# Kernel tuning notes

Measured on AMD Instinct MI355X. Metric: run time of the kernel, lower is better.

Reference implementation:

```python
import jax, jax.numpy as jnp
import numpy as np
import math

B, L, S = 2, 2048, 2048
DIN, DK, DV, DOUT, H = 512, 512, 512, 512, 8
HEAD_SIZE = DK / H  # attention_head_size = dim_key_query_all / num_attention_heads


def setup_inputs() -> dict:
    key = jax.random.key(0)
    ks = jax.random.split(key, 12)
    inv = 1.0 / math.sqrt(DIN)
    return {
        "queries": jax.random.normal(ks[0], (B, L, DIN), jnp.float32),
        "keys": jax.random.normal(ks[1], (B, S, DIN), jnp.float32),
        "values": jax.random.normal(ks[2], (B, S, DIN), jnp.float32),
        "attn_mask": 0,
        "Wq": jax.random.uniform(ks[3], (DK, DIN), jnp.float32, -inv, inv),
        "Wk": jax.random.uniform(ks[4], (DK, DIN), jnp.float32, -inv, inv),
        "Wv": jax.random.uniform(ks[5], (DV, DIN), jnp.float32, -inv, inv),
        "bv": jax.random.uniform(ks[6], (DV,), jnp.float32, -inv, inv),
        "Wcb": jax.random.uniform(ks[7], (H, DIN), jnp.float32, -inv, inv),
        "mixing": 0.2 * jax.random.normal(ks[8], (H, DK), jnp.float32),
        "Wd": jax.random.uniform(ks[9], (DOUT, DV), jnp.float32, -1.0 / math.sqrt(DV), 1.0 / math.sqrt(DV)),
        "bd": jax.random.uniform(ks[10], (DOUT,), jnp.float32, -1.0 / math.sqrt(DV), 1.0 / math.sqrt(DV)),
    }


def reference(queries, keys, values, attn_mask, Wq, Wk, Wv, bv, Wcb, mixing, Wd, bd):
    # projections
    q = jnp.einsum('bld,ed->ble', queries, Wq)            # [B,L,DK]
    k = jnp.einsum('bsd,ed->bse', keys, Wk)               # [B,S,DK]
    v = jnp.einsum('bsd,ed->bse', values, Wv) + bv        # [B,S,DV]
    v = v.reshape(B, S, H, DV // H).transpose(0, 2, 1, 3)  # [B,H,S,dv]
    # collaborative scores: (q * mixing_h) @ k^T, per head
    mixed_q = q[:, None, :, :] * mixing[None, :, None, :]  # [B,H,L,DK]
    scores = jnp.einsum('bhle,bse->bhls', mixed_q, k)      # [B,H,L,S]
    # content bias: keys -> [B,S,H] -> broadcast over queries
    cb = jnp.einsum('bsd,hd->bhs', keys, Wcb)              # [B,H,S]
    scores = (scores + cb[:, :, None, :]) / math.sqrt(HEAD_SIZE)
    probs = jax.nn.softmax(scores, axis=-1)                # dropout p=0 (eval)
    ctx = jnp.einsum('bhls,bhsv->bhlv', probs, v)          # [B,H,L,dv]
    ctx = ctx.transpose(0, 2, 1, 3).reshape(B, L, DV)      # [B,L,DV]
    out = jnp.einsum('blv,ov->blo', ctx, Wd) + bd          # [B,L,DOUT]
    return out, probs
```

## Files before the change

### kernel.cpp

```cpp
#include <hip/hip_runtime.h>

typedef unsigned short u16;
typedef __bf16 bf16x8 __attribute__((ext_vector_type(8)));
typedef float floatx4 __attribute__((ext_vector_type(4)));

#define B_ 2
#define L_ 2048
#define S_ 2048
#define D_ 512
#define H_ 8

static __device__ __forceinline__ u16 f2bf(float f) {
  union { float f; unsigned u; } v; v.f = f;
  unsigned u = v.u;
  return (u16)((u + 0x7FFFu + ((u >> 16) & 1u)) >> 16);
}
static __device__ __forceinline__ float bf2f(u16 h) {
  union { unsigned u; float f; } v; v.u = ((unsigned)h) << 16;
  return v.f;
}

static __device__ __forceinline__ void gload16(const void* g, void* l) {
  __builtin_amdgcn_global_load_lds(
      (const __attribute__((address_space(1))) void*)g,
      (__attribute__((address_space(3))) void*)l, 16, 0, 0);
}

__global__ __launch_bounds__(256) void qkv_gemm(
    const float* __restrict__ Qin, const float* __restrict__ Kin, const float* __restrict__ Vin,
    const float* __restrict__ Wq, const float* __restrict__ Wk, const float* __restrict__ Wv,
    const float* __restrict__ bv,
    u16* __restrict__ qo, u16* __restrict__ ko, u16* __restrict__ vo)
{
  __shared__ u16 As[128][72];
  __shared__ u16 Bs[128][72];
  const int z = blockIdx.z;
  const float* A = (z == 0) ? Qin : (z == 1) ? Kin : Vin;
  const float* W = (z == 0) ? Wq : (z == 1) ? Wk : Wv;
  const int tid = threadIdx.x;
  const int m0 = blockIdx.y * 128;
  const int n0 = blockIdx.x * 128;
  const int lane = tid & 63, w = tid >> 6;
  const int ml = lane & 15, kl = lane >> 4;
  const int mqw = (w >> 1) * 64, nq = (w & 1) * 64;
  const int srow = tid >> 4, scg = tid & 15;

  floatx4 acc[4][4] = {};

  for (int k0 = 0; k0 < 512; k0 += 64) {
#pragma unroll
    for (int i = 0; i < 8; ++i) {
      const int r = srow + i * 16;
      float4 av = *(const float4*)&A[(size_t)(m0 + r) * 512 + k0 + scg * 4];
      ushort4 ua; ua.x = f2bf(av.x); ua.y = f2bf(av.y); ua.z = f2bf(av.z); ua.w = f2bf(av.w);
      *(ushort4*)&As[r][scg * 4] = ua;
      float4 wv = *(const float4*)&W[(size_t)(n0 + r) * 512 + k0 + scg * 4];
      ushort4 uw; uw.x = f2bf(wv.x); uw.y = f2bf(wv.y); uw.z = f2bf(wv.z); uw.w = f2bf(wv.w);
      *(ushort4*)&Bs[r][scg * 4] = uw;
    }
    __syncthreads();
#pragma unroll
    for (int kk = 0; kk < 64; kk += 32) {
      bf16x8 af[4], bfv[4];
#pragma unroll
      for (int i = 0; i < 4; ++i) af[i] = *(const bf16x8*)&As[mqw + i * 16 + ml][kk + kl * 8];
#pragma unroll
      for (int j = 0; j < 4; ++j) bfv[j] = *(const bf16x8*)&Bs[nq + j * 16 + ml][kk + kl * 8];
#pragma unroll
      for (int i = 0; i < 4; ++i)
#pragma unroll
        for (int j = 0; j < 4; ++j)
          acc[i][j] = __builtin_amdgcn_mfma_f32_16x16x32_bf16(af[i], bfv[j], acc[i][j], 0, 0, 0);
    }
    __syncthreads();
  }
#pragma unroll
  for (int i = 0; i < 4; ++i)
#pragma unroll
    for (int j = 0; j < 4; ++j) {
      const int gc = n0 + nq + j * 16 + ml;
#pragma unroll
      for (int r = 0; r < 4; ++r) {
        const int gr = m0 + mqw + i * 16 + kl * 4 + r;
        float v = acc[i][j][r];
        if (z == 0)      qo[(size_t)gr * 512 + gc] = f2bf(v);
        else if (z == 1) ko[(size_t)gr * 512 + gc] = f2bf(v);
        else             vo[(size_t)gr * 512 + gc] = f2bf(v + bv[gc]);
      }
    }
}

__global__ __launch_bounds__(256) void mixq_kernel(
    const u16* __restrict__ qb, const float* __restrict__ mixing, u16* __restrict__ mq)
{
  __shared__ float mixs[8 * 512];
  const int tid = threadIdx.x;
#pragma unroll
  for (int i = 0; i < 4; ++i)
    *(float4*)&mixs[(tid + i * 256) * 4] = *(const float4*)&mixing[(tid + i * 256) * 4];
  __syncthreads();
  const size_t unit = (size_t)blockIdx.x * 256 + tid;
  const size_t el = unit * 8;
  const int e = (int)(el & 511);
  const size_t bl = el >> 9;
  const int b = (int)(bl >> 11);
  const int l = (int)(bl & 2047);
  uint4 qv = *(const uint4*)&qb[el];
  const float q0 = bf2f((u16)(qv.x & 0xFFFFu)), q1 = bf2f((u16)(qv.x >> 16));
  const float q2 = bf2f((u16)(qv.y & 0xFFFFu)), q3 = bf2f((u16)(qv.y >> 16));
  const float q4 = bf2f((u16)(qv.z & 0xFFFFu)), q5 = bf2f((u16)(qv.z >> 16));
  const float q6 = bf2f((u16)(qv.w & 0xFFFFu)), q7 = bf2f((u16)(qv.w >> 16));
#pragma unroll
  for (int h = 0; h < 8; ++h) {
    const float* mp = &mixs[h * 512 + e];
    uint4 o;
    o.x = (unsigned)f2bf(q0 * mp[0]) | ((unsigned)f2bf(q1 * mp[1]) << 16);
    o.y = (unsigned)f2bf(q2 * mp[2]) | ((unsigned)f2bf(q3 * mp[3]) << 16);
    o.z = (unsigned)f2bf(q4 * mp[4]) | ((unsigned)f2bf(q5 * mp[5]) << 16);
    o.w = (unsigned)f2bf(q6 * mp[6]) | ((unsigned)f2bf(q7 * mp[7]) << 16);
    *(uint4*)&mq[(((size_t)b * 8 + h) * 2048 + l) * 512 + e] = o;
  }
}

__global__ __launch_bounds__(256) void out_gemm(
    const float* __restrict__ A, const float* __restrict__ W,
    const float* __restrict__ bias, float* __restrict__ out)
{
  __shared__ u16 As[128][72];
  __shared__ u16 Bs[128][72];
  const int tid = threadIdx.x;
  const int m0 = blockIdx.y * 128;
  const int n0 = blockIdx.x * 128;
  const int lane = tid & 63, w = tid >> 6;
  const int ml = lane & 15, kl = lane >> 4;
  const int mqw = (w >> 1) * 64, nq = (w & 1) * 64;
  const int srow = tid >> 4, scg = tid & 15;

  floatx4 acc[4][4] = {};

  for (int k0 = 0; k0 < 512; k0 += 64) {
#pragma unroll
    for (int i = 0; i < 8; ++i) {
      const int r = srow + i * 16;
      float4 av = *(const float4*)&A[(size_t)(m0 + r) * 512 + k0 + scg * 4];
      ushort4 ua; ua.x = f2bf(av.x); ua.y = f2bf(av.y); ua.z = f2bf(av.z); ua.w = f2bf(av.w);
      *(ushort4*)&As[r][scg * 4] = ua;
      float4 wv = *(const float4*)&W[(size_t)(n0 + r) * 512 + k0 + scg * 4];
      ushort4 uw; uw.x = f2bf(wv.x); uw.y = f2bf(wv.y); uw.z = f2bf(wv.z); uw.w = f2bf(wv.w);
      *(ushort4*)&Bs[r][scg * 4] = uw;
    }
    __syncthreads();
#pragma unroll
    for (int kk = 0; kk < 64; kk += 32) {
      bf16x8 af[4], bfv[4];
#pragma unroll
      for (int i = 0; i < 4; ++i) af[i] = *(const bf16x8*)&As[mqw + i * 16 + ml][kk + kl * 8];
#pragma unroll
      for (int j = 0; j < 4; ++j) bfv[j] = *(const bf16x8*)&Bs[nq + j * 16 + ml][kk + kl * 8];
#pragma unroll
      for (int i = 0; i < 4; ++i)
#pragma unroll
        for (int j = 0; j < 4; ++j)
          acc[i][j] = __builtin_amdgcn_mfma_f32_16x16x32_bf16(af[i], bfv[j], acc[i][j], 0, 0, 0);
    }
    __syncthreads();
  }
#pragma unroll
  for (int i = 0; i < 4; ++i)
#pragma unroll
    for (int j = 0; j < 4; ++j) {
      const int gc = n0 + nq + j * 16 + ml;
#pragma unroll
      for (int r = 0; r < 4; ++r) {
        const int gr = m0 + mqw + i * 16 + kl * 4 + r;
        out[(size_t)gr * 512 + gc] = acc[i][j][r] + bias[gc];
      }
    }
}

__global__ __launch_bounds__(256) void cb_kernel(
    const float* __restrict__ keys, const float* __restrict__ Wcb, float* __restrict__ cbuf)
{
  __shared__ float Wl[8 * 512];
  const int tid = threadIdx.x;
#pragma unroll
  for (int i = 0; i < 4; ++i) {
    const int idx = tid + i * 256;
    *(float4*)&Wl[idx * 4] = *(const float4*)&Wcb[idx * 4];
  }
  __syncthreads();
  const int w = tid >> 6, lane = tid & 63;
  const int rowid = blockIdx.x * 4 + w;
  const int b = rowid >> 11, s = rowid & 2047;
  const float* kr = keys + (size_t)rowid * 512;
  float acc[8] = {0.f, 0.f, 0.f, 0.f, 0.f, 0.f, 0.f, 0.f};
  for (int e = lane; e < 512; e += 64) {
    const float kv = kr[e];
#pragma unroll
    for (int hh = 0; hh < 8; ++hh) acc[hh] += kv * Wl[hh * 512 + e];
  }
#pragma unroll
  for (int hh = 0; hh < 8; ++hh) {
#pragma unroll
    for (int off = 32; off > 0; off >>= 1) acc[hh] += __shfl_xor(acc[hh], off, 64);
  }
  if (lane == 0) {
#pragma unroll
    for (int hh = 0; hh < 8; ++hh)
      cbuf[((size_t)b * 8 + hh) * 2048 + s] = acc[hh];
  }
}

__global__ __launch_bounds__(256) void transpose_v(
    const u16* __restrict__ vb, u16* __restrict__ vT)
{
  __shared__ u16 t[64][72];
  const int tid = threadIdx.x;
  const int e0 = blockIdx.x * 64;
  const int s0 = blockIdx.y * 64;
  const int b = blockIdx.z;
  const int rr = tid >> 3, g = tid & 7;
#pragma unroll
  for (int i = 0; i < 2; ++i) {
    const int r = rr + i * 32;
    *(uint4*)&t[r][g * 8] = *(const uint4*)&vb[((size_t)b * S_ + s0 + r) * 512 + e0 + g * 8];
  }
  __syncthreads();
#pragma unroll
  for (int i = 0; i < 2; ++i) {
    const int er = rr + i * 32;
    uint4 o;
    o.x = (unsigned)t[g * 8 + 0][er] | ((unsigned)t[g * 8 + 1][er] << 16);
    o.y = (unsigned)t[g * 8 + 2][er] | ((unsigned)t[g * 8 + 3][er] << 16);
    o.z = (unsigned)t[g * 8 + 4][er] | ((unsigned)t[g * 8 + 5][er] << 16);
    o.w = (unsigned)t[g * 8 + 6][er] | ((unsigned)t[g * 8 + 7][er] << 16);
    *(uint4*)&vT[((size_t)b * 512 + e0 + er) * S_ + s0 + g * 8] = o;
  }
}

template<int BF16OUT>
__global__ __launch_bounds__(256) void scores_gemm(
    const u16* __restrict__ mq, const u16* __restrict__ kb,
    const float* __restrict__ cbuf, float* __restrict__ sc, u16* __restrict__ sb)
{
  __shared__ u16 As[128][64];
  __shared__ u16 Bs[128][64];
  const int tid = threadIdx.x;
  const int bh = blockIdx.z, b = bh >> 3;
  const int m0 = blockIdx.y * 128;
  const int n0 = blockIdx.x * 128;
  const u16* mqb = mq + (size_t)bh * L_ * 512;
  const u16* kbb = kb + (size_t)b * S_ * 512;
  const int lane = tid & 63, w = tid >> 6;
  const int ml = lane & 15, kl = lane >> 4;
  const int mqw = (w >> 1) * 64, nq = (w & 1) * 64;
  const int lr = lane >> 3;
  const int lc = (lane & 7) * 8;

  floatx4 acc[4][4] = {};

  for (int k0 = 0; k0 < 512; k0 += 64) {
#pragma unroll
    for (int i = 0; i < 4; ++i) {
      const int c = w * 4 + i;
      const int r = c * 8 + lr;
      gload16(&mqb[(size_t)(m0 + r) * 512 + k0 + lc], &As[c * 8][0]);
      gload16(&kbb[(size_t)(n0 + r) * 512 + k0 + lc], &Bs[c * 8][0]);
    }
    __syncthreads();
#pragma unroll
    for (int kk = 0; kk < 64; kk += 32) {
      bf16x8 af[4], bfv[4];
#pragma unroll
      for (int i = 0; i < 4; ++i) af[i] = *(const bf16x8*)&As[mqw + i * 16 + ml][kk + kl * 8];
#pragma unroll
      for (int j = 0; j < 4; ++j) bfv[j] = *(const bf16x8*)&Bs[nq + j * 16 + ml][kk + kl * 8];
#pragma unroll
      for (int i = 0; i < 4; ++i)
#pragma unroll
        for (int j = 0; j < 4; ++j)
          acc[i][j] = __builtin_amdgcn_mfma_f32_16x16x32_bf16(af[i], bfv[j], acc[i][j], 0, 0, 0);
    }
    __syncthreads();
  }
  if constexpr (BF16OUT) {
    u16* outp = sb + ((size_t)bh * L_ + m0) * S_ + n0;
#pragma unroll
    for (int j = 0; j < 4; ++j) {
      const int gcl = nq + j * 16 + ml;
      const float cbv = cbuf[(size_t)bh * S_ + n0 + gcl];
#pragma unroll
      for (int i = 0; i < 4; ++i)
#pragma unroll
        for (int r = 0; r < 4; ++r) {
          const int grl = mqw + i * 16 + kl * 4 + r;
          outp[(size_t)grl * S_ + gcl] = f2bf((acc[i][j][r] + cbv) * 0.125f);
        }
    }
  } else {
    float* outp = sc + ((size_t)bh * L_ + m0) * S_ + n0;
#pragma unroll
    for (int j = 0; j < 4; ++j) {
      const int gcl = nq + j * 16 + ml;
      const float cbv = cbuf[(size_t)bh * S_ + n0 + gcl];
#pragma unroll
      for (int i = 0; i < 4; ++i)
#pragma unroll
        for (int r = 0; r < 4; ++r) {
          const int grl = mqw + i * 16 + kl * 4 + r;
          outp[(size_t)grl * S_ + gcl] = (acc[i][j][r] + cbv) * 0.125f;
        }
    }
  }
}

template<int BF16IN>
__global__ __launch_bounds__(256) void softmax_stream(
    u16* __restrict__ sb, float* probs)
{
  const int tid = threadIdx.x;
  const int row = blockIdx.x * 4 + (tid >> 6);
  const int lane = tid & 63;
  float s[32];
  if constexpr (BF16IN) {
    const u16* rp = sb + (size_t)row * 2048;
#pragma unroll
    for (int j = 0; j < 8; ++j) {
      uint2 v = *(const uint2*)&rp[lane * 4 + j * 256];
      s[4 * j + 0] = bf2f((u16)(v.x & 0xFFFFu));
      s[4 * j + 1] = bf2f((u16)(v.x >> 16));
      s[4 * j + 2] = bf2f((u16)(v.y & 0xFFFFu));
      s[4 * j + 3] = bf2f((u16)(v.y >> 16));
    }
  } else {
    const float* rp = probs + (size_t)row * 2048;
#pragma unroll
    for (int j = 0; j < 8; ++j) {
      float4 v = *(const float4*)&rp[lane * 4 + j * 256];
      s[4 * j + 0] = v.x; s[4 * j + 1] = v.y; s[4 * j + 2] = v.z; s[4 * j + 3] = v.w;
    }
  }
  float m = -3.0e38f;
#pragma unroll
  for (int i = 0; i < 32; ++i) m = fmaxf(m, s[i]);
#pragma unroll
  for (int off = 32; off > 0; off >>= 1) m = fmaxf(m, __shfl_xor(m, off, 64));
  float s0 = 0.f, s1 = 0.f, s2 = 0.f, s3 = 0.f;
#pragma unroll
  for (int i = 0; i < 32; i += 4) {
    s[i + 0] = __expf(s[i + 0] - m); s0 += s[i + 0];
    s[i + 1] = __expf(s[i + 1] - m); s1 += s[i + 1];
    s[i + 2] = __expf(s[i + 2] - m); s2 += s[i + 2];
    s[i + 3] = __expf(s[i + 3] - m); s3 += s[i + 3];
  }
  float sum = (s0 + s1) + (s2 + s3);
#pragma unroll
  for (int off = 32; off > 0; off >>= 1) sum += __shfl_xor(sum, off, 64);
  const float rl = 1.0f / sum;
  float* op = probs + (size_t)row * 2048;
  u16* bp = sb + (size_t)row * 2048;
#pragma unroll
  for (int j = 0; j < 8; ++j) {
    float4 o;
    o.x = s[4 * j + 0] * rl; o.y = s[4 * j + 1] * rl;
    o.z = s[4 * j + 2] * rl; o.w = s[4 * j + 3] * rl;
    *(float4*)&op[lane * 4 + j * 256] = o;
    if constexpr (BF16IN) {
      uint2 t;
      t.x = (unsigned)f2bf(o.x) | ((unsigned)f2bf(o.y) << 16);
      t.y = (unsigned)f2bf(o.z) | ((unsigned)f2bf(o.w) << 16);
      *(uint2*)&bp[lane * 4 + j * 256] = t;
    }
  }
}

template<int BF16IN>
__global__ __launch_bounds__(256) void ctx_gemm(
    const float* __restrict__ probsf, const u16* __restrict__ pb,
    const u16* __restrict__ vT, float* __restrict__ ctx)
{
  __shared__ u16 As[64][64];
  __shared__ u16 Bs[64][64];
  const int tid = threadIdx.x;
  const int bh = blockIdx.y, b = bh >> 3, h = bh & 7;
  const int m0 = blockIdx.x * 64;
  const int lane = tid & 63, w = tid >> 6;
  const int ml = lane & 15, kl = lane >> 4;
  const int lr = lane >> 3;
  const int lc = (lane & 7) * 8;
  const u16* Ap = pb + ((size_t)bh * L_ + m0) * S_;
  const u16* Bp = vT + ((size_t)b * 512 + h * 64) * S_;

  floatx4 acc[4] = {};

  for (int k0 = 0; k0 < 2048; k0 += 64) {
    if constexpr (BF16IN) {
#pragma unroll
      for (int i = 0; i < 2; ++i) {
        const int c = w * 2 + i;
        const int r = c * 8 + lr;
        gload16(&Ap[(size_t)r * S_ + k0 + lc], &As[c * 8][0]);
        gload16(&Bp[(size_t)r * S_ + k0 + lc], &Bs[c * 8][0]);
      }
    } else {
      const int srow = tid >> 4, scg = tid & 15;
#pragma unroll
      for (int i = 0; i < 4; ++i) {
        const int r = srow + i * 16;
        float4 av = *(const float4*)&probsf[((size_t)bh * L_ + m0 + r) * S_ + k0 + scg * 4];
        ushort4 ua; ua.x = f2bf(av.x); ua.y = f2bf(av.y); ua.z = f2bf(av.z); ua.w = f2bf(av.w);
        *(ushort4*)&As[r][scg * 4] = ua;
      }
#pragma unroll
      for (int i = 0; i < 2; ++i) {
        const int c = w * 2 + i;
        const int r = c * 8 + lr;
        gload16(&Bp[(size_t)r * S_ + k0 + lc], &Bs[c * 8][0]);
      }
    }
    __syncthreads();
#pragma unroll
    for (int kk = 0; kk < 64; kk += 32) {
      bf16x8 af = *(const bf16x8*)&As[w * 16 + ml][kk + kl * 8];
#pragma unroll
      for (int j = 0; j < 4; ++j) {
        bf16x8 bfv = *(const bf16x8*)&Bs[j * 16 + ml][kk + kl * 8];
        acc[j] = __builtin_amdgcn_mfma_f32_16x16x32_bf16(af, bfv, acc[j], 0, 0, 0);
      }
    }
    __syncthreads();
  }
#pragma unroll
  for (int j = 0; j < 4; ++j) {
    const int gc = h * 64 + j * 16 + ml;
#pragma unroll
    for (int r = 0; r < 4; ++r) {
      const int gl = m0 + w * 16 + kl * 4 + r;
      ctx[((size_t)b * L_ + gl) * 512 + gc] = acc[j][r];
    }
  }
}

extern "C" void kernel_launch(void* const* d_in, const int* in_sizes, int n_in,
                              void* d_out, int out_size, void* d_ws, size_t ws_size,
                              hipStream_t stream) {
  const float* queries = (const float*)d_in[0];
  const float* keys    = (const float*)d_in[1];
  const float* values  = (const float*)d_in[2];
  const float* Wq  = (const float*)d_in[4];
  const float* Wk  = (const float*)d_in[5];
  const float* Wv  = (const float*)d_in[6];
  const float* bv  = (const float*)d_in[7];
  const float* Wcb = (const float*)d_in[8];
  const float* mixing = (const float*)d_in[9];
  const float* Wd  = (const float*)d_in[10];
  const float* bd  = (const float*)d_in[11];

  float* out   = (float*)d_out;
  float* probs = out + (size_t)B_ * L_ * 512;

  char* ws = (char*)d_ws;
  u16*   qb  = (u16*)(ws);
  u16*   kb  = (u16*)(ws + (size_t)4  * 1024 * 1024);
  u16*   vb  = (u16*)(ws + (size_t)8  * 1024 * 1024);
  u16*   vT  = (u16*)(ws + (size_t)12 * 1024 * 1024);
  float* cbuf= (float*)(ws + (size_t)16 * 1024 * 1024);
  float* ctx = (float*)(ws + (size_t)17 * 1024 * 1024);
  u16*   mq  = (u16*)(ws + (size_t)25 * 1024 * 1024);
  const size_t SB16_OFF = (size_t)57 * 1024 * 1024;
  const size_t SB16_SZ  = (size_t)B_ * H_ * L_ * S_ * 2;
  u16* sb16 = (u16*)(ws + SB16_OFF);
  const bool bigws = (ws_size >= SB16_OFF + SB16_SZ);

  hipLaunchKernelGGL(qkv_gemm, dim3(4, 32, 3), dim3(256), 0, stream,
                     queries, keys, values, Wq, Wk, Wv, bv, qb, kb, vb);
  hipLaunchKernelGGL(mixq_kernel, dim3(1024), dim3(256), 0, stream, qb, mixing, mq);
  hipLaunchKernelGGL(cb_kernel, dim3(1024), dim3(256), 0, stream, keys, Wcb, cbuf);
  hipLaunchKernelGGL(transpose_v, dim3(8, 32, 2), dim3(256), 0, stream, vb, vT);
  if (bigws) {
    hipLaunchKernelGGL(HIP_KERNEL_NAME(scores_gemm<1>), dim3(16, 16, 16), dim3(256), 0, stream,
                       mq, kb, cbuf, probs, sb16);
    hipLaunchKernelGGL(HIP_KERNEL_NAME(softmax_stream<1>), dim3(8192), dim3(256), 0, stream,
                       sb16, probs);
    hipLaunchKernelGGL(HIP_KERNEL_NAME(ctx_gemm<1>), dim3(32, 16), dim3(256), 0, stream,
                       probs, sb16, vT, ctx);
  } else {
    hipLaunchKernelGGL(HIP_KERNEL_NAME(scores_gemm<0>), dim3(16, 16, 16), dim3(256), 0, stream,
                       mq, kb, cbuf, probs, sb16);
    hipLaunchKernelGGL(HIP_KERNEL_NAME(softmax_stream<0>), dim3(8192), dim3(256), 0, stream,
                       sb16, probs);
    hipLaunchKernelGGL(HIP_KERNEL_NAME(ctx_gemm<0>), dim3(32, 16), dim3(256), 0, stream,
                       probs, sb16, vT, ctx);
  }
  hipLaunchKernelGGL(out_gemm, dim3(4, 32, 1), dim3(256), 0, stream,
                     ctx, Wd, bd, out);
}
```

Before: 579.6 us.

## Split-K the context GEMM and fuse content-bias with V transpose

The probs·V GEMM is split into two K-halves over a new grid dimension, doubling the block count. Each half writes its own partial context buffer, and the output GEMM sums the two partials while staging its A tile. The content-bias kernel and the V transpose kernel are merged into one launch that branches on block index, removing one launch. In exchange the bf16 path now needs an extra 8 MB of workspace, and if the workspace is too small it falls back to the fp32 path.

```diff
diff --git a/kernel.cpp b/kernel.cpp
--- a/kernel.cpp
+++ b/kernel.cpp
@@ -123,7 +123,8 @@
 }
 
 __global__ __launch_bounds__(256) void out_gemm(
-    const float* __restrict__ A, const float* __restrict__ W,
+    const float* __restrict__ A0, const float* __restrict__ A1,
+    const float* __restrict__ W,
     const float* __restrict__ bias, float* __restrict__ out)
 {
   __shared__ u16 As[128][72];
@@ -142,8 +143,12 @@
 #pragma unroll
     for (int i = 0; i < 8; ++i) {
       const int r = srow + i * 16;
-      float4 av = *(const float4*)&A[(size_t)(m0 + r) * 512 + k0 + scg * 4];
-      ushort4 ua; ua.x = f2bf(av.x); ua.y = f2bf(av.y); ua.z = f2bf(av.z); ua.w = f2bf(av.w);
+      const size_t aoff = (size_t)(m0 + r) * 512 + k0 + scg * 4;
+      float4 a0 = *(const float4*)&A0[aoff];
+      float4 a1 = *(const float4*)&A1[aoff];
+      ushort4 ua;
+      ua.x = f2bf(a0.x + a1.x); ua.y = f2bf(a0.y + a1.y);
+      ua.z = f2bf(a0.z + a1.z); ua.w = f2bf(a0.w + a1.w);
       *(ushort4*)&As[r][scg * 4] = ua;
       float4 wv = *(const float4*)&W[(size_t)(n0 + r) * 512 + k0 + scg * 4];
       ushort4 uw; uw.x = f2bf(wv.x); uw.y = f2bf(wv.y); uw.z = f2bf(wv.z); uw.w = f2bf(wv.w);
@@ -178,63 +183,63 @@
     }
 }
 
-__global__ __launch_bounds__(256) void cb_kernel(
-    const float* __restrict__ keys, const float* __restrict__ Wcb, float* __restrict__ cbuf)
+__global__ __launch_bounds__(256) void prep_kernel(
+    const float* __restrict__ keys, const float* __restrict__ Wcb, float* __restrict__ cbuf,
+    const u16* __restrict__ vb, u16* __restrict__ vT)
 {
   __shared__ float Wl[8 * 512];
-  const int tid = threadIdx.x;
-#pragma unroll
-  for (int i = 0; i < 4; ++i) {
-    const int idx = tid + i * 256;
-    *(float4*)&Wl[idx * 4] = *(const float4*)&Wcb[idx * 4];
-  }
-  __syncthreads();
-  const int w = tid >> 6, lane = tid & 63;
-  const int rowid = blockIdx.x * 4 + w;
-  const int b = rowid >> 11, s = rowid & 2047;
-  const float* kr = keys + (size_t)rowid * 512;
-  float acc[8] = {0.f, 0.f, 0.f, 0.f, 0.f, 0.f, 0.f, 0.f};
-  for (int e = lane; e < 512; e += 64) {
-    const float kv = kr[e];
-#pragma unroll
-    for (int hh = 0; hh < 8; ++hh) acc[hh] += kv * Wl[hh * 512 + e];
-  }
-#pragma unroll
-  for (int hh = 0; hh < 8; ++hh) {
-#pragma unroll
-    for (int off = 32; off > 0; off >>= 1) acc[hh] += __shfl_xor(acc[hh], off, 64);
-  }
-  if (lane == 0) {
-#pragma unroll
-    for (int hh = 0; hh < 8; ++hh)
-      cbuf[((size_t)b * 8 + hh) * 2048 + s] = acc[hh];
-  }
-}
-
-__global__ __launch_bounds__(256) void transpose_v(
-    const u16* __restrict__ vb, u16* __restrict__ vT)
-{
   __shared__ u16 t[64][72];
   const int tid = threadIdx.x;
-  const int e0 = blockIdx.x * 64;
-  const int s0 = blockIdx.y * 64;
-  const int b = blockIdx.z;
-  const int rr = tid >> 3, g = tid & 7;
-#pragma unroll
-  for (int i = 0; i < 2; ++i) {
-    const int r = rr + i * 32;
-    *(uint4*)&t[r][g * 8] = *(const uint4*)&vb[((size_t)b * S_ + s0 + r) * 512 + e0 + g * 8];
-  }
-  __syncthreads();
-#pragma unroll
-  for (int i = 0; i < 2; ++i) {
-    const int er = rr + i * 32;
-    uint4 o;
-    o.x = (unsigned)t[g * 8 + 0][er] | ((unsigned)t[g * 8 + 1][er] << 16);
-    o.y = (unsigned)t[g * 8 + 2][er] | ((unsigned)t[g * 8 + 3][er] << 16);
-    o.z = (unsigned)t[g * 8 + 4][er] | ((unsigned)t[g * 8 + 5][er] << 16);
-    o.w = (unsigned)t[g * 8 + 6][er] | ((unsigned)t[g * 8 + 7][er] << 16);
-    *(uint4*)&vT[((size_t)b * 512 + e0 + er) * S_ + s0 + g * 8] = o;
+  if (blockIdx.x < 1024) {
+#pragma unroll
+    for (int i = 0; i < 4; ++i) {
+      const int idx = tid + i * 256;
+      *(float4*)&Wl[idx * 4] = *(const float4*)&Wcb[idx * 4];
+    }
+    __syncthreads();
+    const int w = tid >> 6, lane = tid & 63;
+    const int rowid = blockIdx.x * 4 + w;
+    const int b = rowid >> 11, s = rowid & 2047;
+    const float* kr = keys + (size_t)rowid * 512;
+    float acc[8] = {0.f, 0.f, 0.f, 0.f, 0.f, 0.f, 0.f, 0.f};
+    for (int e = lane; e < 512; e += 64) {
+      const float kv = kr[e];
+#pragma unroll
+      for (int hh = 0; hh < 8; ++hh) acc[hh] += kv * Wl[hh * 512 + e];
+    }
+#pragma unroll
+    for (int hh = 0; hh < 8; ++hh) {
+#pragma unroll
+      for (int off = 32; off > 0; off >>= 1) acc[hh] += __shfl_xor(acc[hh], off, 64);
+    }
+    if (lane == 0) {
+#pragma unroll
+      for (int hh = 0; hh < 8; ++hh)
+        cbuf[((size_t)b * 8 + hh) * 2048 + s] = acc[hh];
+    }
+  } else {
+    const int id = blockIdx.x - 1024;
+    const int b = id >> 8;
+    const int rem = id & 255;
+    const int s0 = (rem >> 3) * 64;
+    const int e0 = (rem & 7) * 64;
+    const int rr = tid >> 3, g = tid & 7;
+#pragma unroll
+    for (int i = 0; i < 2; ++i) {
+      const int r = rr + i * 32;
+      *(uint4*)&t[r][g * 8] = *(const uint4*)&vb[((size_t)b * S_ + s0 + r) * 512 + e0 + g * 8];
+    }
+    __syncthreads();
+#pragma unroll
+    for (int i = 0; i < 2; ++i) {
+      const int er = rr + i * 32;
+      uint4 o;
+      o.x = (unsigned)t[g * 8 + 0][er] | ((unsigned)t[g * 8 + 1][er] << 16);
+      o.y = (unsigned)t[g * 8 + 2][er] | ((unsigned)t[g * 8 + 3][er] << 16);
+      o.z = (unsigned)t[g * 8 + 4][er] | ((unsigned)t[g * 8 + 5][er] << 16);
+      o.w = (unsigned)t[g * 8 + 6][er] | ((unsigned)t[g * 8 + 7][er] << 16);
+      *(uint4*)&vT[((size_t)b * 512 + e0 + er) * S_ + s0 + g * 8] = o;
+    }
   }
 }
 
@@ -377,12 +382,13 @@
 template<int BF16IN>
 __global__ __launch_bounds__(256) void ctx_gemm(
     const float* __restrict__ probsf, const u16* __restrict__ pb,
-    const u16* __restrict__ vT, float* __restrict__ ctx)
+    const u16* __restrict__ vT, float* __restrict__ ctx0, float* __restrict__ ctx1)
 {
   __shared__ u16 As[64][64];
   __shared__ u16 Bs[64][64];
   const int tid = threadIdx.x;
-  const int bh = blockIdx.y, b = bh >> 3, h = bh & 7;
+  const int kz = blockIdx.y;
+  const int bh = blockIdx.z, b = bh >> 3, h = bh & 7;
   const int m0 = blockIdx.x * 64;
   const int lane = tid & 63, w = tid >> 6;
   const int ml = lane & 15, kl = lane >> 4;
@@ -393,7 +399,8 @@
 
   floatx4 acc[4] = {};
 
-  for (int k0 = 0; k0 < 2048; k0 += 64) {
+  const int kend = kz * 1024 + 1024;
+  for (int k0 = kz * 1024; k0 < kend; k0 += 64) {
     if constexpr (BF16IN) {
 #pragma unroll
       for (int i = 0; i < 2; ++i) {
@@ -430,13 +437,14 @@
     }
     __syncthreads();
   }
+  float* cdst = kz ? ctx1 : ctx0;
 #pragma unroll
   for (int j = 0; j < 4; ++j) {
     const int gc = h * 64 + j * 16 + ml;
 #pragma unroll
     for (int r = 0; r < 4; ++r) {
       const int gl = m0 + w * 16 + kl * 4 + r;
-      ctx[((size_t)b * L_ + gl) * 512 + gc] = acc[j][r];
+      cdst[((size_t)b * L_ + gl) * 512 + gc] = acc[j][r];
     }
   }
 }
@@ -465,33 +473,35 @@
   u16*   vb  = (u16*)(ws + (size_t)8  * 1024 * 1024);
   u16*   vT  = (u16*)(ws + (size_t)12 * 1024 * 1024);
   float* cbuf= (float*)(ws + (size_t)16 * 1024 * 1024);
-  float* ctx = (float*)(ws + (size_t)17 * 1024 * 1024);
+  float* ctx0= (float*)(ws + (size_t)17 * 1024 * 1024);
   u16*   mq  = (u16*)(ws + (size_t)25 * 1024 * 1024);
   const size_t SB16_OFF = (size_t)57 * 1024 * 1024;
   const size_t SB16_SZ  = (size_t)B_ * H_ * L_ * S_ * 2;
   u16* sb16 = (u16*)(ws + SB16_OFF);
-  const bool bigws = (ws_size >= SB16_OFF + SB16_SZ);
+  const bool bigws = (ws_size >= SB16_OFF + SB16_SZ + (size_t)8 * 1024 * 1024);
+  float* ctx1 = bigws ? (float*)(ws + SB16_OFF + SB16_SZ)
+                      : (float*)(ws + SB16_OFF);
 
   hipLaunchKernelGGL(qkv_gemm, dim3(4, 32, 3), dim3(256), 0, stream,
                      queries, keys, values, Wq, Wk, Wv, bv, qb, kb, vb);
   hipLaunchKernelGGL(mixq_kernel, dim3(1024), dim3(256), 0, stream, qb, mixing, mq);
-  hipLaunchKernelGGL(cb_kernel, dim3(1024), dim3(256), 0, stream, keys, Wcb, cbuf);
-  hipLaunchKernelGGL(transpose_v, dim3(8, 32, 2), dim3(256), 0, stream, vb, vT);
+  hipLaunchKernelGGL(prep_kernel, dim3(1536), dim3(256), 0, stream,
+                     keys, Wcb, cbuf, vb, vT);
   if (bigws) {
     hipLaunchKernelGGL(HIP_KERNEL_NAME(scores_gemm<1>), dim3(16, 16, 16), dim3(256), 0, stream,
                        mq, kb, cbuf, probs, sb16);
     hipLaunchKernelGGL(HIP_KERNEL_NAME(softmax_stream<1>), dim3(8192), dim3(256), 0, stream,
                        sb16, probs);
-    hipLaunchKernelGGL(HIP_KERNEL_NAME(ctx_gemm<1>), dim3(32, 16), dim3(256), 0, stream,
-                       probs, sb16, vT, ctx);
+    hipLaunchKernelGGL(HIP_KERNEL_NAME(ctx_gemm<1>), dim3(32, 2, 16), dim3(256), 0, stream,
+                       probs, sb16, vT, ctx0, ctx1);
   } else {
     hipLaunchKernelGGL(HIP_KERNEL_NAME(scores_gemm<0>), dim3(16, 16, 16), dim3(256), 0, stream,
                        mq, kb, cbuf, probs, sb16);
     hipLaunchKernelGGL(HIP_KERNEL_NAME(softmax_stream<0>), dim3(8192), dim3(256), 0, stream,
                        sb16, probs);
-    hipLaunchKernelGGL(HIP_KERNEL_NAME(ctx_gemm<0>), dim3(32, 16), dim3(256), 0, stream,
-                       probs, sb16, vT, ctx);
+    hipLaunchKernelGGL(HIP_KERNEL_NAME(ctx_gemm<0>), dim3(32, 2, 16), dim3(256), 0, stream,
+                       probs, sb16, vT, ctx0, ctx1);
   }
   hipLaunchKernelGGL(out_gemm, dim3(4, 32, 1), dim3(256), 0, stream,
-                     ctx, Wd, bd, out);
-}
+                     ctx0, ctx1, Wd, bd, out);
+}
```

Result: faster. 563.5 us (-2.8%).
